# Performance work log

Measured on AMD Instinct MI355X. Metric: run time of the kernel, lower is better.

Reference implementation:

```python
import jax, jax.numpy as jnp
import numpy as np

# ---- shape constants (d_data=1, expand_factor=1) ----
B, L, DD = 32, 8192, 1
M, NL = 3, 2                      # 3 Mamba control nets, n_layers=2 each
DM = 4 * DD                       # mamba d_model = 4*d_data
DI = DM                           # d_inner = expand_factor * d_model
NS = 16                           # d_state
KC = 4                            # d_conv
DR = max(1, -(-DM // 16))         # dt_rank = ceil(d_model/16)
DT = 1e-4                         # forward scalar arg dt (fixed python float)
TAU = 1000.0
SMOOTH = int(round(0.001 / DT))   # smooth_len/dt = 10

# 9-point (8th order) central finite-difference coefficients for f' (no 1/dt)
_C1 = [1/280, -4/105, 1/5, -4/5, 0.0, 4/5, -1/5, 4/105, -1/280]

def deriv_approx_dy(x):
    Lp = x.shape[1] - 8
    return sum(c * x[:, k:k + Lp, :] for k, c in enumerate(_C1) if c != 0.0)

def smooth(x, k):
    # centered box filter, same output length (via cumsum sliding window)
    if k <= 1:
        return x
    xp = jnp.pad(x, ((0, 0), ((k - 1) // 2 + 1, k // 2), (0, 0)))
    c = jnp.cumsum(xp, axis=1)
    return (c[:, k:, :] - c[:, :-k, :]) / k

def rmsnorm(x, w):
    return x * jax.lax.rsqrt(jnp.mean(x * x, -1, keepdims=True) + 1e-5) * w

def causal_conv(u, w, b):
    # depthwise causal conv == torch Conv1d(groups=DI, padding=KC-1)[..., :L]
    Lc = u.shape[1]
    up = jnp.pad(u, ((0, 0), (KC - 1, 0), (0, 0)))
    y = sum(up[:, j:j + Lc, :] * w[:, j] for j in range(KC))
    return y + b

def selective_scan(u, delta, A, Bm, Cm, Dp):
    # u, delta: [b,l,di]; A: [di,ns]; Bm, Cm: [b,l,ns]; Dp: [di]
    dA = jnp.exp(delta[..., None] * A)                         # [b,l,di,ns]
    dBu = delta[..., None] * Bm[:, :, None, :] * u[..., None]  # [b,l,di,ns]
    def step(h, xs):
        a, bu = xs
        h = a * h + bu
        return h, h
    h0 = jnp.zeros((u.shape[0], DI, NS), u.dtype)
    _, hs = jax.lax.scan(step, h0, (jnp.moveaxis(dA, 1, 0), jnp.moveaxis(dBu, 1, 0)))
    hs = jnp.moveaxis(hs, 0, 1)                                # [b,l,di,ns]
    return jnp.einsum('bldn,bln->bld', hs, Cm) + u * Dp

def _run_mamba(x_in, m, in_proj_w, conv_w, conv_b, x_proj_w,
               dt_proj_w, dt_proj_b, A_log, D_param, norm_w, out_proj_w):
    h = x_in
    for l in range(NL):
        hn = rmsnorm(h, norm_w[m, l])
        xz = hn @ in_proj_w[m, l].T                            # [b,l,2*di]
        xc, res = jnp.split(xz, 2, axis=-1)
        xc = jax.nn.silu(causal_conv(xc, conv_w[m, l], conv_b[m, l]))
        dbc = xc @ x_proj_w[m, l].T
        dtr, Bm, Cm = dbc[..., :DR], dbc[..., DR:DR + NS], dbc[..., DR + NS:]
        delta = jax.nn.softplus(dtr @ dt_proj_w[m, l].T + dt_proj_b[m, l])
        A = -jnp.exp(A_log[m, l])
        y = selective_scan(xc, delta, A, Bm, Cm, D_param[m, l])
        y = y * jax.nn.silu(res)
        h = y @ out_proj_w[m, l].T + h                         # residual block
    return h

def _forward(x, in_proj_w, conv_w, conv_b, x_proj_w, dt_proj_w, dt_proj_b,
             A_log, D_param, norm_w, out_proj_w, omega_w, omega_b,
             gamma_w, gamma_b, d_w, d_b, b_param):
    xdot = deriv_approx_dy(x)                                  # [B, L-8, DD]
    z = jnp.concatenate([x[:, 4:-4, :], xdot], axis=-1)        # [B, L', 2]
    x_in = jnp.concatenate([z, jnp.flip(z, axis=1)], axis=-1)  # [B, L', 4]
    args = (in_proj_w, conv_w, conv_b, x_proj_w, dt_proj_w, dt_proj_b,
            A_log, D_param, norm_w, out_proj_w)
    omegaC = _run_mamba(x_in, 0, *args)
    gammaC = _run_mamba(x_in, 1, *args)
    dC = _run_mamba(x_in, 2, *args)
    b = jax.nn.relu(b_param) / TAU
    d = jax.nn.relu(dC @ d_w.T + d_b)
    omega = omegaC @ omega_w.T + omega_b
    gamma = (gammaC @ gamma_w.T + gamma_b) / TAU
    d = smooth(jnp.abs(d), SMOOTH)
    omega = smooth(jnp.abs(omega), SMOOTH)
    gamma = smooth(gamma, SMOOTH)
    z = jnp.concatenate([z[:, :, :-1], z[:, :, -1:] / DT], axis=-1)
    z1, z2 = z[:, :, :1], z[:, :, 1:]
    yhat = -omega ** 2 * z1 + gamma * z2 - b * (z1 ** 2) * z2 - d
    def pen(t):
        # torch.var(dim=1) is unbiased -> ddof=1
        return jnp.mean(jnp.var(jnp.diff(t, axis=1)[:, 1:, :], axis=1, ddof=1))
    penalty = (pen(omega) + pen(gamma) + pen(d)) / 3.0
    controls = jnp.concatenate([omegaC, gammaC, dC], axis=-1)
    return yhat, controls, penalty

def setup_inputs():
    key = jax.random.key(0)
    ks = jax.random.split(key, 16)
    f32 = jnp.float32
    def nrm(k, shape, s=0.1):
        return s * jax.random.normal(k, shape, f32)
    x = jax.random.normal(ks[0], (B, L, DD), f32)
    A_log = jnp.log(jnp.broadcast_to(jnp.arange(1, NS + 1, dtype=f32), (M, NL, DI, NS)))
    return {
        "x": x,
        "in_proj_w": nrm(ks[1], (M, NL, 2 * DI, DM)),
        "conv_w": nrm(ks[2], (M, NL, DI, KC)),
        "conv_b": nrm(ks[3], (M, NL, DI)),
        "x_proj_w": nrm(ks[4], (M, NL, DR + 2 * NS, DI)),
        "dt_proj_w": nrm(ks[5], (M, NL, DI, DR)),
        "dt_proj_b": nrm(ks[6], (M, NL, DI)),
        "A_log": A_log,
        "D_param": jnp.ones((M, NL, DI), f32),
        "norm_w": jnp.ones((M, NL, DM), f32),
        "out_proj_w": nrm(ks[7], (M, NL, DM, DI)),
        "omega_w": nrm(ks[8], (DD, DM)),
        "omega_b": nrm(ks[9], (DD,)),
        "gamma_w": nrm(ks[10], (DD, DM)),
        "gamma_b": nrm(ks[11], (DD,)),
        "d_w": nrm(ks[12], (DD, DM)),
        "d_b": nrm(ks[13], (DD,)),
        "b_param": jax.random.uniform(ks[14], (1,), f32),
    }

def reference(x, in_proj_w, conv_w, conv_b, x_proj_w, dt_proj_w, dt_proj_b,
              A_log, D_param, norm_w, out_proj_w, omega_w, omega_b,
              gamma_w, gamma_b, d_w, d_b, b_param):
    return _forward(x, in_proj_w, conv_w, conv_b, x_proj_w, dt_proj_w, dt_proj_b,
                    A_log, D_param, norm_w, out_proj_w, omega_w, omega_b,
                    gamma_w, gamma_b, d_w, d_b, b_param)
```

## Files before the change

### kernel.cpp

```cpp
#include <hip/hip_runtime.h>
#include <math.h>

#define Bn_   32
#define Ln_   8192
#define LCn   8184
#define NLn   2
#define NCHn  341
#define CHn   24
#define NGn   24

static constexpr long N_BL = (long)Bn_ * LCn;

static constexpr long OFF_H    = 0;
static constexpr long OFF_REC  = 12*N_BL;
static constexpr long OFF_YB   = 36*N_BL;
static constexpr long OFF_RAW  = OFF_REC;
static constexpr long OFF_PART = OFF_REC + 3*N_BL;

#define L2E_  1.4426950408889634f
#define LN2_  0.6931471805599453f
#define EXP2_(x) __builtin_amdgcn_exp2f(x)
#define LOG2_(x) __builtin_amdgcn_logf(x)

__device__ __forceinline__ float si_(float v) {
    float e = EXP2_(-v * L2E_);
    return v * __builtin_amdgcn_rcpf(1.f + e);
}

__device__ __forceinline__ float sel4(float4 v, int d) {
    return (d & 2) ? ((d & 1) ? v.w : v.z) : ((d & 1) ? v.y : v.x);
}

__device__ __forceinline__ float rowsum16(float p) {
    p += __int_as_float(__builtin_amdgcn_update_dpp(0, __float_as_int(p), 0x128, 0xF, 0xF, true));
    p += __int_as_float(__builtin_amdgcn_update_dpp(0, __float_as_int(p), 0x124, 0xF, 0xF, true));
    p += __int_as_float(__builtin_amdgcn_update_dpp(0, __float_as_int(p), 0x122, 0xF, 0xF, true));
    p += __int_as_float(__builtin_amdgcn_update_dpp(0, __float_as_int(p), 0x121, 0xF, 0xF, true));
    return p;
}

__device__ __forceinline__ float4 compute_xin(const float* __restrict__ xb, int p) {
    const float c0 = 1.f/280.f, c1 = -4.f/105.f, c2 = 0.2f, c3 = -0.8f,
                c5 = 0.8f, c6 = -0.2f, c7 = 4.f/105.f, c8 = -1.f/280.f;
    float xd  = c0*xb[p]   + c1*xb[p+1] + c2*xb[p+2] + c3*xb[p+3]
              + c5*xb[p+5] + c6*xb[p+6] + c7*xb[p+7] + c8*xb[p+8];
    int tf = LCn - 1 - p;
    float xdf = c0*xb[tf]   + c1*xb[tf+1] + c2*xb[tf+2] + c3*xb[tf+3]
              + c5*xb[tf+5] + c6*xb[tf+6] + c7*xb[tf+7] + c8*xb[tf+8];
    float4 v; v.x = xb[p+4]; v.y = xd; v.z = xb[tf+4]; v.w = xdf;
    return v;
}

__device__ __forceinline__ float4 rms_xproj(float4 hv, const float* __restrict__ wn,
                                            const float* __restrict__ W) {
    float ms = (hv.x*hv.x + hv.y*hv.y + hv.z*hv.z + hv.w*hv.w)*0.25f + 1e-5f;
    float rs = __builtin_amdgcn_rsqf(ms);
    float hn0 = hv.x*rs*wn[0], hn1 = hv.y*rs*wn[1];
    float hn2 = hv.z*rs*wn[2], hn3 = hv.w*rs*wn[3];
    float4 o;
    o.x = W[0]*hn0  + W[1]*hn1  + W[2]*hn2  + W[3]*hn3;
    o.y = W[4]*hn0  + W[5]*hn1  + W[6]*hn2  + W[7]*hn3;
    o.z = W[8]*hn0  + W[9]*hn1  + W[10]*hn2 + W[11]*hn3;
    o.w = W[12]*hn0 + W[13]*hn1 + W[14]*hn2 + W[15]*hn3;
    return o;
}

__device__ __forceinline__ void conv_lg_store(const float4* xp, int k, int ml,
                                              const float* __restrict__ cw,
                                              const float* __restrict__ cbv,
                                              const float* __restrict__ xpw,
                                              const float* __restrict__ dtw,
                                              const float* __restrict__ dtb,
                                              float* __restrict__ rp) {
    const float* wc = cw  + ml*16;
    const float* bc = cbv + ml*4;
    float acc0 = bc[0], acc1 = bc[1], acc2 = bc[2], acc3 = bc[3];
#pragma unroll
    for (int j = 0; j < 4; j++) {
        float4 xv = xp[k + j];
        acc0 = fmaf(xv.x, wc[0*4+j], acc0);
        acc1 = fmaf(xv.y, wc[1*4+j], acc1);
        acc2 = fmaf(xv.z, wc[2*4+j], acc2);
        acc3 = fmaf(xv.w, wc[3*4+j], acc3);
    }
    float4 o;
    o.x = si_(acc0); o.y = si_(acc1); o.z = si_(acc2); o.w = si_(acc3);
    const float* P = xpw + (long)ml*33*4;
    float dtr = o.x*P[0] + o.y*P[1] + o.z*P[2] + o.w*P[3];
    const float* dwv = dtw + ml*4;
    const float* dbv = dtb + ml*4;
    float4 lg;
    lg.x = LOG2_(1.f + EXP2_(fmaf(dtr, dwv[0], dbv[0]) * L2E_));
    lg.y = LOG2_(1.f + EXP2_(fmaf(dtr, dwv[1], dbv[1]) * L2E_));
    lg.z = LOG2_(1.f + EXP2_(fmaf(dtr, dwv[2], dbv[2]) * L2E_));
    lg.w = LOG2_(1.f + EXP2_(fmaf(dtr, dwv[3], dbv[3]) * L2E_));
    *(float4*)rp       = o;
    *(float4*)(rp + 4) = lg;
}

__global__ __launch_bounds__(256)
void k_pre0(const float* __restrict__ x,
            const float* __restrict__ ipw, const float* __restrict__ cw,
            const float* __restrict__ cbv, const float* __restrict__ nw,
            const float* __restrict__ xpw, const float* __restrict__ dtw,
            const float* __restrict__ dtb, float* __restrict__ rec) {
    __shared__ float4 xp[259];
    int blk = blockIdx.x;
    int m = blk >> 10, bb = (blk >> 5) & 31, tile = blk & 31;
    int ml = m*NLn;
    int t0 = tile << 8, k = threadIdx.x;
    int t  = t0 + k;
    const float* xb = x + (long)bb*Ln_;
    const float* W  = ipw + (long)ml*32;
    const float* wn = nw  + ml*4;
    auto G = [&](int p) -> float4 {
        float4 o; o.x = o.y = o.z = o.w = 0.f;
        if (p >= 0 && p < LCn) o = rms_xproj(compute_xin(xb, p), wn, W);
        return o;
    };
    xp[k + 3] = G(t);
    if (k < 3) xp[k] = G(t0 + k - 3);
    __syncthreads();
    if (t >= LCn) return;
    conv_lg_store(xp, k, ml, cw, cbv, xpw, dtw, dtb,
                  rec + ((long)m*N_BL + (long)bb*LCn + t)*8);
}

__global__ __launch_bounds__(256)
void k_mid(const float* __restrict__ x, const float* __restrict__ yb,
           float* __restrict__ hout,
           const float* __restrict__ ipw, const float* __restrict__ cw,
           const float* __restrict__ cbv, const float* __restrict__ nw,
           const float* __restrict__ xpw, const float* __restrict__ dtw,
           const float* __restrict__ dtb, const float* __restrict__ opw,
           float* __restrict__ rec) {
    __shared__ float4 xp[259];
    int blk = blockIdx.x;
    int m = blk >> 10, bb = (blk >> 5) & 31, tile = blk & 31;
    int ml0 = m*NLn, ml1 = ml0 + 1;
    int t0 = tile << 8, k = threadIdx.x;
    int t  = t0 + k;
    const float* xb  = x + (long)bb*Ln_;
    const float* wn0 = nw + ml0*4;
    const float* Wr  = ipw + (long)(ml0*8 + 4)*4;
    const float* O   = opw + ml0*16;
    const float* wn1 = nw + ml1*4;
    const float* W1  = ipw + (long)ml1*32;
    auto H = [&](int p) -> float4 {
        float4 hv = compute_xin(xb, p);
        float ms = (hv.x*hv.x + hv.y*hv.y + hv.z*hv.z + hv.w*hv.w)*0.25f + 1e-5f;
        float rs = __builtin_amdgcn_rsqf(ms);
        float hn0 = hv.x*rs*wn0[0], hn1 = hv.y*rs*wn0[1];
        float hn2 = hv.z*rs*wn0[2], hn3 = hv.w*rs*wn0[3];
        float4 yv = *(const float4*)(yb + ((long)m*N_BL + (long)bb*LCn + p)*4);
        float g0 = yv.x * si_(Wr[0]*hn0  + Wr[1]*hn1  + Wr[2]*hn2  + Wr[3]*hn3);
        float g1 = yv.y * si_(Wr[4]*hn0  + Wr[5]*hn1  + Wr[6]*hn2  + Wr[7]*hn3);
        float g2 = yv.z * si_(Wr[8]*hn0  + Wr[9]*hn1  + Wr[10]*hn2 + Wr[11]*hn3);
        float g3 = yv.w * si_(Wr[12]*hn0 + Wr[13]*hn1 + Wr[14]*hn2 + Wr[15]*hn3);
        float4 o;
        o.x = O[0]*g0  + O[1]*g1  + O[2]*g2  + O[3]*g3  + hv.x;
        o.y = O[4]*g0  + O[5]*g1  + O[6]*g2  + O[7]*g3  + hv.y;
        o.z = O[8]*g0  + O[9]*g1  + O[10]*g2 + O[11]*g3 + hv.z;
        o.w = O[12]*g0 + O[13]*g1 + O[14]*g2 + O[15]*g3 + hv.w;
        return o;
    };
    float4 zf; zf.x = zf.y = zf.z = zf.w = 0.f;
    if (t < LCn) {
        float4 hnew = H(t);
        *(float4*)(hout + ((long)m*N_BL + (long)bb*LCn + t)*4) = hnew;
        xp[k + 3] = rms_xproj(hnew, wn1, W1);
    } else {
        xp[k + 3] = zf;
    }
    if (k < 3) {
        int p = t0 + k - 3;
        xp[k] = (p >= 0) ? rms_xproj(H(p), wn1, W1) : zf;
    }
    __syncthreads();
    if (t >= LCn) return;
    conv_lg_store(xp, k, ml1, cw, cbv, xpw, dtw, dtb,
                  rec + ((long)m*N_BL + (long)bb*LCn + t)*8);
}

__global__ __launch_bounds__(256, 8)
void k_scanB(const float* __restrict__ rec, int l,
             const float* __restrict__ xpw, const float* __restrict__ Alog,
             float* __restrict__ Ap, float* __restrict__ Sv) {
    int wid  = blockIdx.x*4 + (threadIdx.x >> 6);
    int lane = threadIdx.x & 63;
    int chunk = wid % NCHn;
    int g     = wid / NCHn;
    int m = g >> 3;
    int s = lane >> 4, n = lane & 15;
    int bb = (g & 7)*4 + s;
    int ml = m*NLn + l;
    const float* P  = xpw + (long)ml*33*4;
    const float* PB = P + (1+n)*4;
    float pb0 = PB[0]*LN2_, pb1 = PB[1]*LN2_, pb2 = PB[2]*LN2_, pb3 = PB[3]*LN2_;
    const float* AL = Alog + (long)ml*64 + n;
    float4 Av;
    Av.x = -EXP2_(AL[0]  * L2E_);
    Av.y = -EXP2_(AL[16] * L2E_);
    Av.z = -EXP2_(AL[32] * L2E_);
    Av.w = -EXP2_(AL[48] * L2E_);
    const float* rb = rec + ((long)m*N_BL + (long)bb*LCn)*8;
    int t0 = chunk*CHn;
    float4 ap; ap.x = ap.y = ap.z = ap.w = 1.f;
    float4 sv; sv.x = sv.y = sv.z = sv.w = 0.f;
#pragma unroll 4
    for (int t = t0; t < t0 + CHn; t++) {
        float4 u  = *(const float4*)(rb + (long)t*8);
        float4 lg = *(const float4*)(rb + (long)t*8 + 4);
        float Bv = u.x*pb0 + u.y*pb1 + u.z*pb2 + u.w*pb3;
        float4 a;
        a.x = EXP2_(lg.x * Av.x); a.y = EXP2_(lg.y * Av.y);
        a.z = EXP2_(lg.z * Av.z); a.w = EXP2_(lg.w * Av.w);
        sv.x = fmaf(a.x, sv.x, lg.x*u.x*Bv);
        sv.y = fmaf(a.y, sv.y, lg.y*u.y*Bv);
        sv.z = fmaf(a.z, sv.z, lg.z*u.z*Bv);
        sv.w = fmaf(a.w, sv.w, lg.w*u.w*Bv);
        ap.x *= a.x; ap.y *= a.y; ap.z *= a.z; ap.w *= a.w;
    }
    long ci = (((long)g*NCHn + chunk)*64 + lane)*4;
    *(float4*)(Ap + ci) = ap;
    *(float4*)(Sv + ci) = sv;
}

#define SCANC_G 8
__global__ __launch_bounds__(256)
void k_scanC(const float* __restrict__ Ap, float* __restrict__ Sv) {
    int g   = blockIdx.x;
    int tid = threadIdx.x;
    long base = (long)g*NCHn*256 + tid;
    const int NFULL = NCHn / SCANC_G;
    float h = 0.f;
    float ca[SCANC_G], cs[SCANC_G], na[SCANC_G], ns[SCANC_G];
#pragma unroll
    for (int j = 0; j < SCANC_G; j++) {
        ca[j] = Ap[base + (long)j*256];
        cs[j] = Sv[base + (long)j*256];
    }
    for (int grp = 0; grp < NFULL; grp++) {
        long gb = base + (long)grp*SCANC_G*256;
        if (grp + 1 < NFULL) {
            long nb = gb + (long)SCANC_G*256;
#pragma unroll
            for (int j = 0; j < SCANC_G; j++) {
                na[j] = Ap[nb + (long)j*256];
                ns[j] = Sv[nb + (long)j*256];
            }
        }
#pragma unroll
        for (int j = 0; j < SCANC_G; j++) {
            Sv[gb + (long)j*256] = h;
            h = fmaf(ca[j], h, cs[j]);
        }
#pragma unroll
        for (int j = 0; j < SCANC_G; j++) { ca[j] = na[j]; cs[j] = ns[j]; }
    }
    for (int cc = NFULL*SCANC_G; cc < NCHn; cc++) {
        long ci = base + (long)cc*256;
        float a = Ap[ci];
        float s = Sv[ci];
        Sv[ci] = h;
        h = fmaf(a, h, s);
    }
}

__global__ __launch_bounds__(256, 8)
void k_scanD(const float* __restrict__ rec, float* __restrict__ yb, int l,
             const float* __restrict__ xpw, const float* __restrict__ Alog,
             const float* __restrict__ H0, const float* __restrict__ Dp) {
    int wid  = blockIdx.x*4 + (threadIdx.x >> 6);
    int lane = threadIdx.x & 63;
    int chunk = wid % NCHn;
    int g     = wid / NCHn;
    int m = g >> 3;
    int s = lane >> 4, n = lane & 15;
    int bb = (g & 7)*4 + s;
    int ml = m*NLn + l;
    const float* P  = xpw + (long)ml*33*4;
    const float* PB = P + (1+n)*4;
    float pb0 = PB[0]*LN2_, pb1 = PB[1]*LN2_, pb2 = PB[2]*LN2_, pb3 = PB[3]*LN2_;
    const float* PC = P + (17+n)*4;
    float pc0 = PC[0], pc1 = PC[1], pc2 = PC[2], pc3 = PC[3];
    const float* AL = Alog + (long)ml*64 + n;
    float4 Av;
    Av.x = -EXP2_(AL[0]  * L2E_);
    Av.y = -EXP2_(AL[16] * L2E_);
    Av.z = -EXP2_(AL[32] * L2E_);
    Av.w = -EXP2_(AL[48] * L2E_);
    float Dd = Dp[ml*4 + (n & 3)];
    float4 h = *(const float4*)(H0 + (((long)g*NCHn + chunk)*64 + lane)*4);
    const float* rb = rec + ((long)m*N_BL + (long)bb*LCn)*8;
    float* ym = yb + ((long)m*N_BL + (long)bb*LCn)*4;
    int t0 = chunk*CHn;
#pragma unroll 4
    for (int t = t0; t < t0 + CHn; t++) {
        float4 u  = *(const float4*)(rb + (long)t*8);
        float4 lg = *(const float4*)(rb + (long)t*8 + 4);
        float Bv = u.x*pb0 + u.y*pb1 + u.z*pb2 + u.w*pb3;
        float Cv = u.x*pc0 + u.y*pc1 + u.z*pc2 + u.w*pc3;
        float4 a;
        a.x = EXP2_(lg.x * Av.x); a.y = EXP2_(lg.y * Av.y);
        a.z = EXP2_(lg.z * Av.z); a.w = EXP2_(lg.w * Av.w);
        h.x = fmaf(a.x, h.x, lg.x*u.x*Bv);
        h.y = fmaf(a.y, h.y, lg.y*u.y*Bv);
        h.z = fmaf(a.z, h.z, lg.z*u.z*Bv);
        h.w = fmaf(a.w, h.w, lg.w*u.w*Bv);
        float px = rowsum16(h.x * Cv);
        float py = rowsum16(h.y * Cv);
        float pz = rowsum16(h.z * Cv);
        float pw = rowsum16(h.w * Cv);
        if (n < 4) {
            float out = (n & 2) ? ((n & 1) ? pw : pz) : ((n & 1) ? py : px);
            float ud  = sel4(u, n);
            ym[(long)t*4 + n] = fmaf(ud, Dd, out);
        }
    }
}

__global__ void k_postHead(const float* __restrict__ hin,
                           const float* __restrict__ yb,
                           const float* __restrict__ ipw, const float* __restrict__ nw,
                           const float* __restrict__ opw,
                           const float* __restrict__ ww, const float* __restrict__ wb,
                           const float* __restrict__ gw, const float* __restrict__ gb,
                           const float* __restrict__ dw, const float* __restrict__ dbp,
                           float* __restrict__ raw, float* __restrict__ dout) {
    long r = (long)blockIdx.x * 256 + threadIdx.x;
    if (r >= N_BL) return;
    float4 om[3];
#pragma unroll
    for (int m = 0; m < 3; m++) {
        int ml = m*NLn + 1;
        float4 hv = *(const float4*)(hin + (long)m*4*N_BL + r*4);
        float ms = (hv.x*hv.x + hv.y*hv.y + hv.z*hv.z + hv.w*hv.w)*0.25f + 1e-5f;
        float rs = __builtin_amdgcn_rsqf(ms);
        const float* wn = nw + ml*4;
        float hn0 = hv.x*rs*wn[0], hn1 = hv.y*rs*wn[1];
        float hn2 = hv.z*rs*wn[2], hn3 = hv.w*rs*wn[3];
        const float* W = ipw + (long)(ml*8 + 4)*4;
        float4 yv = *(const float4*)(yb + ((long)m*N_BL + r)*4);
        float g0 = yv.x * si_(W[0]*hn0  + W[1]*hn1  + W[2]*hn2  + W[3]*hn3);
        float g1 = yv.y * si_(W[4]*hn0  + W[5]*hn1  + W[6]*hn2  + W[7]*hn3);
        float g2 = yv.z * si_(W[8]*hn0  + W[9]*hn1  + W[10]*hn2 + W[11]*hn3);
        float g3 = yv.w * si_(W[12]*hn0 + W[13]*hn1 + W[14]*hn2 + W[15]*hn3);
        const float* O = opw + ml*16;
        float4 o;
        o.x = O[0]*g0  + O[1]*g1  + O[2]*g2  + O[3]*g3  + hv.x;
        o.y = O[4]*g0  + O[5]*g1  + O[6]*g2  + O[7]*g3  + hv.y;
        o.z = O[8]*g0  + O[9]*g1  + O[10]*g2 + O[11]*g3 + hv.z;
        o.w = O[12]*g0 + O[13]*g1 + O[14]*g2 + O[15]*g3 + hv.w;
        om[m] = o;
    }
    float4* c = (float4*)(dout + N_BL + r*12);
    c[0] = om[0]; c[1] = om[1]; c[2] = om[2];
    raw[r]          = om[0].x*ww[0] + om[0].y*ww[1] + om[0].z*ww[2] + om[0].w*ww[3] + wb[0];
    raw[N_BL + r]   = (om[1].x*gw[0] + om[1].y*gw[1] + om[1].z*gw[2] + om[1].w*gw[3] + gb[0]) / 1000.0f;
    raw[2*N_BL + r] = fmaxf(om[2].x*dw[0] + om[2].y*dw[1] + om[2].z*dw[2] + om[2].w*dw[3] + dbp[0], 0.f);
}

__global__ __launch_bounds__(256)
void k_smoothpen(const float* __restrict__ x, const float* __restrict__ raw,
                 const float* __restrict__ bp, float* __restrict__ dout,
                 double* __restrict__ part) {
    int b    = blockIdx.x >> 5;
    int tile = blockIdx.x & 31;
    int k    = threadIdx.x;
    int t0   = tile << 8;
    int t    = t0 + k;
    __shared__ float so_[257], sg_[257], sd_[257];
    const float* ro = raw + (long)b*LCn;
    const float* rg = raw + N_BL   + (long)b*LCn;
    const float* rd = raw + 2*N_BL + (long)b*LCn;
    auto smo3 = [&](int tt, float& o, float& g, float& d) {
        o = g = d = 0.f;
        if (tt < 0 || tt >= LCn) return;
        int lo = max(tt - 4, 0), hi = min(tt + 5, LCn - 1);
        for (int q = lo; q <= hi; q++) {
            o += fabsf(ro[q]); g += rg[q]; d += fabsf(rd[q]);
        }
        o *= 0.1f; g *= 0.1f; d *= 0.1f;
    };
    float so, sg, sd;
    smo3(t, so, sg, sd);
    so_[k] = so; sg_[k] = sg; sd_[k] = sd;
    if (k == 0) {
        float a, bq, cq;
        smo3(t0 + 256, a, bq, cq);
        so_[256] = a; sg_[256] = bq; sd_[256] = cq;
    }
    __syncthreads();
    if (t < LCn) {
        const float* xb = x + (long)b * Ln_;
        const float c0 = 1.f/280.f, c1 = -4.f/105.f, c2 = 0.2f, c3 = -0.8f,
                    c5 = 0.8f, c6 = -0.2f, c7 = 4.f/105.f, c8 = -1.f/280.f;
        float xd  = c0*xb[t]   + c1*xb[t+1] + c2*xb[t+2] + c3*xb[t+3]
                  + c5*xb[t+5] + c6*xb[t+6] + c7*xb[t+7] + c8*xb[t+8];
        float z1 = xb[t+4];
        float z2 = xd / 0.0001f;
        float bq = fmaxf(bp[0], 0.f) / 1000.0f;
        dout[(long)b*LCn + t] = -so*so*z1 + sg*z2 - bq*z1*z1*z2 - sd;
    }
    double v[6] = {0,0,0,0,0,0};
    if (t >= 1 && t <= LCn - 2) {
        double go = (double)so_[k+1] - (double)so_[k];
        double gg = (double)sg_[k+1] - (double)sg_[k];
        double gd = (double)sd_[k+1] - (double)sd_[k];
        v[0] = go; v[1] = go*go;
        v[2] = gg; v[3] = gg*gg;
        v[4] = gd; v[5] = gd*gd;
    }
#pragma unroll
    for (int j = 0; j < 6; j++) {
        for (int off = 32; off > 0; off >>= 1)
            v[j] += __shfl_down(v[j], off, 64);
    }
    __shared__ double wsum[4][6];
    int w = threadIdx.x >> 6;
    if ((threadIdx.x & 63) == 0) {
#pragma unroll
        for (int j = 0; j < 6; j++) wsum[w][j] = v[j];
    }
    __syncthreads();
    if (threadIdx.x == 0) {
        double s[6];
#pragma unroll
        for (int j = 0; j < 6; j++)
            s[j] = wsum[0][j] + wsum[1][j] + wsum[2][j] + wsum[3][j];
        long pb = (((long)0*32 + b)*32 + tile)*2;
        part[pb]   = s[0]; part[pb+1] = s[1];
        pb = (((long)1*32 + b)*32 + tile)*2;
        part[pb]   = s[2]; part[pb+1] = s[3];
        pb = (((long)2*32 + b)*32 + tile)*2;
        part[pb]   = s[4]; part[pb+1] = s[5];
    }
}

__global__ void k_pen2(const double* __restrict__ part, float* __restrict__ pout) {
    int tid = threadIdx.x;
    double var = 0.0;
    if (tid < 96) {
        int which = tid / 32, b = tid % 32;
        double su = 0.0, s2 = 0.0;
        for (int tl = 0; tl < 32; tl++) {
            const double* p = part + (((long)which*32 + b)*32 + tl)*2;
            su += p[0]; s2 += p[1];
        }
        const double N = (double)(LCn - 2);
        var = (s2 - su*su/N) / (N - 1.0);
    }
    __shared__ double sh[128];
    sh[tid] = var;
    __syncthreads();
    for (int o = 64; o > 0; o >>= 1) {
        if (tid < o) sh[tid] += sh[tid + o];
        __syncthreads();
    }
    if (tid == 0) pout[0] = (float)(sh[0] / 96.0);
}

extern "C" void kernel_launch(void* const* d_in, const int* in_sizes, int n_in,
                              void* d_out, int out_size, void* d_ws, size_t ws_size,
                              hipStream_t stream) {
    const float* x    = (const float*)d_in[0];
    const float* ipw  = (const float*)d_in[1];
    const float* cw   = (const float*)d_in[2];
    const float* cbv  = (const float*)d_in[3];
    const float* xpw  = (const float*)d_in[4];
    const float* dtw  = (const float*)d_in[5];
    const float* dtb  = (const float*)d_in[6];
    const float* Alog = (const float*)d_in[7];
    const float* Dp   = (const float*)d_in[8];
    const float* nw   = (const float*)d_in[9];
    const float* opw  = (const float*)d_in[10];
    const float* ww   = (const float*)d_in[11];
    const float* wb   = (const float*)d_in[12];
    const float* gw   = (const float*)d_in[13];
    const float* gb   = (const float*)d_in[14];
    const float* dw   = (const float*)d_in[15];
    const float* dbp  = (const float*)d_in[16];
    const float* bp   = (const float*)d_in[17];

    float* ws   = (float*)d_ws;
    float* h    = ws + OFF_H;
    float* rec  = ws + OFF_REC;
    float* yb   = ws + OFF_YB;
    float* ap   = yb;
    float* raw  = ws + OFF_RAW;
    double* part = (double*)(ws + OFF_PART);
    float* dout = (float*)d_out;
    float* sv  = dout + 4*N_BL;

    hipLaunchKernelGGL(k_pre0, dim3(3072), dim3(256), 0, stream,
                       x, ipw, cw, cbv, nw, xpw, dtw, dtb, rec);
    hipLaunchKernelGGL(k_scanB, dim3(2046), dim3(256), 0, stream,
                       rec, 0, xpw, Alog, ap, sv);
    hipLaunchKernelGGL(k_scanC, dim3(NGn), dim3(256), 0, stream, ap, sv);
    hipLaunchKernelGGL(k_scanD, dim3(2046), dim3(256), 0, stream,
                       rec, yb, 0, xpw, Alog, sv, Dp);
    hipLaunchKernelGGL(k_mid, dim3(3072), dim3(256), 0, stream,
                       x, yb, h, ipw, cw, cbv, nw, xpw, dtw, dtb, opw, rec);
    hipLaunchKernelGGL(k_scanB, dim3(2046), dim3(256), 0, stream,
                       rec, 1, xpw, Alog, ap, sv);
    hipLaunchKernelGGL(k_scanC, dim3(NGn), dim3(256), 0, stream, ap, sv);
    hipLaunchKernelGGL(k_scanD, dim3(2046), dim3(256), 0, stream,
                       rec, yb, 1, xpw, Alog, sv, Dp);
    hipLaunchKernelGGL(k_postHead, dim3(1023), dim3(256), 0, stream,
                       h, yb, ipw, nw, opw, ww, wb, gw, gb, dw, dbp, raw, dout);
    hipLaunchKernelGGL(k_smoothpen, dim3(1024), dim3(256), 0, stream,
                       x, raw, bp, dout, part);
    hipLaunchKernelGGL(k_pen2, dim3(1), dim3(128), 0, stream, part, dout + 13*N_BL);
}
```

Baseline: 177.8 us.

## Fuse chunk-carry scan into scan pass via last-block atomic, fuse head with smoothing

The chunk-carry scan kernel is folded into the per-chunk scan kernel. A global atomic counter per group lets the last finishing block run the sequential carry propagation. Chunking changes to 328 chunks of 25 steps so there are no leftover chunks, with a bound check on the final chunk. The post-head projection is fused into the smoothing/penalty kernel, which recomputes a 10-element halo in shared memory instead of writing and re-reading an intermediate raw buffer. This removes two launches per layer and one global round trip, at the cost of atomics, fences and some redundant halo compute.

```diff
diff --git a/kernel.cpp b/kernel.cpp
--- a/kernel.cpp
+++ b/kernel.cpp
@@ -5,17 +5,18 @@
 #define Ln_   8192
 #define LCn   8184
 #define NLn   2
-#define NCHn  341
-#define CHn   24
+#define NCHn  328
+#define CHn   25
 #define NGn   24
+#define BLKPG 82
 
 static constexpr long N_BL = (long)Bn_ * LCn;
+static constexpr long NCAR = (long)NGn * NCHn * 256;
 
 static constexpr long OFF_H    = 0;
 static constexpr long OFF_REC  = 12*N_BL;
 static constexpr long OFF_YB   = 36*N_BL;
-static constexpr long OFF_RAW  = OFF_REC;
-static constexpr long OFF_PART = OFF_REC + 3*N_BL;
+static constexpr long OFF_PART = OFF_REC;
 
 #define L2E_  1.4426950408889634f
 #define LN2_  0.6931471805599453f
@@ -103,7 +104,9 @@
             const float* __restrict__ ipw, const float* __restrict__ cw,
             const float* __restrict__ cbv, const float* __restrict__ nw,
             const float* __restrict__ xpw, const float* __restrict__ dtw,
-            const float* __restrict__ dtb, float* __restrict__ rec) {
+            const float* __restrict__ dtb, float* __restrict__ rec,
+            int* __restrict__ gcnt) {
+    if (blockIdx.x == 0 && threadIdx.x < NGn) gcnt[threadIdx.x] = 0;
     __shared__ float4 xp[259];
     int blk = blockIdx.x;
     int m = blk >> 10, bb = (blk >> 5) & 31, tile = blk & 31;
@@ -133,7 +136,8 @@
            const float* __restrict__ cbv, const float* __restrict__ nw,
            const float* __restrict__ xpw, const float* __restrict__ dtw,
            const float* __restrict__ dtb, const float* __restrict__ opw,
-           float* __restrict__ rec) {
+           float* __restrict__ rec, int* __restrict__ gcnt) {
+    if (blockIdx.x == 0 && threadIdx.x < NGn) gcnt[threadIdx.x] = 0;
     __shared__ float4 xp[259];
     int blk = blockIdx.x;
     int m = blk >> 10, bb = (blk >> 5) & 31, tile = blk & 31;
@@ -182,10 +186,12 @@
                   rec + ((long)m*N_BL + (long)bb*LCn + t)*8);
 }
 
+#define SCANC_G 8
 __global__ __launch_bounds__(256, 8)
-void k_scanB(const float* __restrict__ rec, int l,
-             const float* __restrict__ xpw, const float* __restrict__ Alog,
-             float* __restrict__ Ap, float* __restrict__ Sv) {
+void k_scanBC(const float* __restrict__ rec, int l,
+              const float* __restrict__ xpw, const float* __restrict__ Alog,
+              float* __restrict__ Ap, float* __restrict__ Sv,
+              int* __restrict__ gcnt) {
     int wid  = blockIdx.x*4 + (threadIdx.x >> 6);
     int lane = threadIdx.x & 63;
     int chunk = wid % NCHn;
@@ -204,11 +210,11 @@
     Av.z = -EXP2_(AL[32] * L2E_);
     Av.w = -EXP2_(AL[48] * L2E_);
     const float* rb = rec + ((long)m*N_BL + (long)bb*LCn)*8;
-    int t0 = chunk*CHn;
+    int t0 = chunk*CHn, t1 = min(t0 + CHn, LCn);
     float4 ap; ap.x = ap.y = ap.z = ap.w = 1.f;
     float4 sv; sv.x = sv.y = sv.z = sv.w = 0.f;
 #pragma unroll 4
-    for (int t = t0; t < t0 + CHn; t++) {
+    for (int t = t0; t < t1; t++) {
         float4 u  = *(const float4*)(rb + (long)t*8);
         float4 lg = *(const float4*)(rb + (long)t*8 + 4);
         float Bv = u.x*pb0 + u.y*pb1 + u.z*pb2 + u.w*pb3;
@@ -224,12 +230,14 @@
     long ci = (((long)g*NCHn + chunk)*64 + lane)*4;
     *(float4*)(Ap + ci) = ap;
     *(float4*)(Sv + ci) = sv;
-}
-
-#define SCANC_G 8
-__global__ __launch_bounds__(256)
-void k_scanC(const float* __restrict__ Ap, float* __restrict__ Sv) {
-    int g   = blockIdx.x;
+    __threadfence();
+    __syncthreads();
+    __shared__ int lastf;
+    if (threadIdx.x == 0)
+        lastf = (atomicAdd(&gcnt[g], 1) == BLKPG - 1);
+    __syncthreads();
+    if (!lastf) return;
+    __threadfence();
     int tid = threadIdx.x;
     long base = (long)g*NCHn*256 + tid;
     const int NFULL = NCHn / SCANC_G;
@@ -258,13 +266,7 @@
 #pragma unroll
         for (int j = 0; j < SCANC_G; j++) { ca[j] = na[j]; cs[j] = ns[j]; }
     }
-    for (int cc = NFULL*SCANC_G; cc < NCHn; cc++) {
-        long ci = base + (long)cc*256;
-        float a = Ap[ci];
-        float s = Sv[ci];
-        Sv[ci] = h;
-        h = fmaf(a, h, s);
-    }
+    if (tid == 0) gcnt[g] = 0;
 }
 
 __global__ __launch_bounds__(256, 8)
@@ -294,9 +296,9 @@
     float4 h = *(const float4*)(H0 + (((long)g*NCHn + chunk)*64 + lane)*4);
     const float* rb = rec + ((long)m*N_BL + (long)bb*LCn)*8;
     float* ym = yb + ((long)m*N_BL + (long)bb*LCn)*4;
-    int t0 = chunk*CHn;
+    int t0 = chunk*CHn, t1 = min(t0 + CHn, LCn);
 #pragma unroll 4
-    for (int t = t0; t < t0 + CHn; t++) {
+    for (int t = t0; t < t1; t++) {
         float4 u  = *(const float4*)(rb + (long)t*8);
         float4 lg = *(const float4*)(rb + (long)t*8 + 4);
         float Bv = u.x*pb0 + u.y*pb1 + u.z*pb2 + u.w*pb3;
@@ -320,78 +322,80 @@
     }
 }
 
-__global__ void k_postHead(const float* __restrict__ hin,
-                           const float* __restrict__ yb,
-                           const float* __restrict__ ipw, const float* __restrict__ nw,
-                           const float* __restrict__ opw,
-                           const float* __restrict__ ww, const float* __restrict__ wb,
-                           const float* __restrict__ gw, const float* __restrict__ gb,
-                           const float* __restrict__ dw, const float* __restrict__ dbp,
-                           float* __restrict__ raw, float* __restrict__ dout) {
-    long r = (long)blockIdx.x * 256 + threadIdx.x;
-    if (r >= N_BL) return;
-    float4 om[3];
-#pragma unroll
-    for (int m = 0; m < 3; m++) {
-        int ml = m*NLn + 1;
-        float4 hv = *(const float4*)(hin + (long)m*4*N_BL + r*4);
-        float ms = (hv.x*hv.x + hv.y*hv.y + hv.z*hv.z + hv.w*hv.w)*0.25f + 1e-5f;
-        float rs = __builtin_amdgcn_rsqf(ms);
-        const float* wn = nw + ml*4;
-        float hn0 = hv.x*rs*wn[0], hn1 = hv.y*rs*wn[1];
-        float hn2 = hv.z*rs*wn[2], hn3 = hv.w*rs*wn[3];
-        const float* W = ipw + (long)(ml*8 + 4)*4;
-        float4 yv = *(const float4*)(yb + ((long)m*N_BL + r)*4);
-        float g0 = yv.x * si_(W[0]*hn0  + W[1]*hn1  + W[2]*hn2  + W[3]*hn3);
-        float g1 = yv.y * si_(W[4]*hn0  + W[5]*hn1  + W[6]*hn2  + W[7]*hn3);
-        float g2 = yv.z * si_(W[8]*hn0  + W[9]*hn1  + W[10]*hn2 + W[11]*hn3);
-        float g3 = yv.w * si_(W[12]*hn0 + W[13]*hn1 + W[14]*hn2 + W[15]*hn3);
-        const float* O = opw + ml*16;
-        float4 o;
-        o.x = O[0]*g0  + O[1]*g1  + O[2]*g2  + O[3]*g3  + hv.x;
-        o.y = O[4]*g0  + O[5]*g1  + O[6]*g2  + O[7]*g3  + hv.y;
-        o.z = O[8]*g0  + O[9]*g1  + O[10]*g2 + O[11]*g3 + hv.z;
-        o.w = O[12]*g0 + O[13]*g1 + O[14]*g2 + O[15]*g3 + hv.w;
-        om[m] = o;
-    }
-    float4* c = (float4*)(dout + N_BL + r*12);
-    c[0] = om[0]; c[1] = om[1]; c[2] = om[2];
-    raw[r]          = om[0].x*ww[0] + om[0].y*ww[1] + om[0].z*ww[2] + om[0].w*ww[3] + wb[0];
-    raw[N_BL + r]   = (om[1].x*gw[0] + om[1].y*gw[1] + om[1].z*gw[2] + om[1].w*gw[3] + gb[0]) / 1000.0f;
-    raw[2*N_BL + r] = fmaxf(om[2].x*dw[0] + om[2].y*dw[1] + om[2].z*dw[2] + om[2].w*dw[3] + dbp[0], 0.f);
-}
-
 __global__ __launch_bounds__(256)
-void k_smoothpen(const float* __restrict__ x, const float* __restrict__ raw,
-                 const float* __restrict__ bp, float* __restrict__ dout,
-                 double* __restrict__ part) {
+void k_tail(const float* __restrict__ x, const float* __restrict__ hin,
+            const float* __restrict__ yb,
+            const float* __restrict__ ipw, const float* __restrict__ nw,
+            const float* __restrict__ opw,
+            const float* __restrict__ ww, const float* __restrict__ wb,
+            const float* __restrict__ gw, const float* __restrict__ gb,
+            const float* __restrict__ dw, const float* __restrict__ dbp,
+            const float* __restrict__ bp,
+            float* __restrict__ dout, double* __restrict__ part) {
     int b    = blockIdx.x >> 5;
     int tile = blockIdx.x & 31;
     int k    = threadIdx.x;
     int t0   = tile << 8;
-    int t    = t0 + k;
+    __shared__ float ro_[266], rg_[266], rd_[266];
     __shared__ float so_[257], sg_[257], sd_[257];
-    const float* ro = raw + (long)b*LCn;
-    const float* rg = raw + N_BL   + (long)b*LCn;
-    const float* rd = raw + 2*N_BL + (long)b*LCn;
-    auto smo3 = [&](int tt, float& o, float& g, float& d) {
+    auto rawcalc = [&](int e) {
+        int t = t0 - 4 + e;
+        float vo = 0.f, vg = 0.f, vd = 0.f;
+        if (t >= 0 && t < LCn) {
+            long r = (long)b*LCn + t;
+            float4 om[3];
+#pragma unroll
+            for (int m = 0; m < 3; m++) {
+                int ml = m*NLn + 1;
+                float4 hv = *(const float4*)(hin + (long)m*4*N_BL + r*4);
+                float ms = (hv.x*hv.x + hv.y*hv.y + hv.z*hv.z + hv.w*hv.w)*0.25f + 1e-5f;
+                float rs = __builtin_amdgcn_rsqf(ms);
+                const float* wn = nw + ml*4;
+                float hn0 = hv.x*rs*wn[0], hn1 = hv.y*rs*wn[1];
+                float hn2 = hv.z*rs*wn[2], hn3 = hv.w*rs*wn[3];
+                const float* W = ipw + (long)(ml*8 + 4)*4;
+                float4 yv = *(const float4*)(yb + ((long)m*N_BL + r)*4);
+                float g0 = yv.x * si_(W[0]*hn0  + W[1]*hn1  + W[2]*hn2  + W[3]*hn3);
+                float g1 = yv.y * si_(W[4]*hn0  + W[5]*hn1  + W[6]*hn2  + W[7]*hn3);
+                float g2 = yv.z * si_(W[8]*hn0  + W[9]*hn1  + W[10]*hn2 + W[11]*hn3);
+                float g3 = yv.w * si_(W[12]*hn0 + W[13]*hn1 + W[14]*hn2 + W[15]*hn3);
+                const float* O = opw + ml*16;
+                float4 o;
+                o.x = O[0]*g0  + O[1]*g1  + O[2]*g2  + O[3]*g3  + hv.x;
+                o.y = O[4]*g0  + O[5]*g1  + O[6]*g2  + O[7]*g3  + hv.y;
+                o.z = O[8]*g0  + O[9]*g1  + O[10]*g2 + O[11]*g3 + hv.z;
+                o.w = O[12]*g0 + O[13]*g1 + O[14]*g2 + O[15]*g3 + hv.w;
+                om[m] = o;
+            }
+            float4* c = (float4*)(dout + N_BL + r*12);
+            c[0] = om[0]; c[1] = om[1]; c[2] = om[2];
+            vo = om[0].x*ww[0] + om[0].y*ww[1] + om[0].z*ww[2] + om[0].w*ww[3] + wb[0];
+            vg = (om[1].x*gw[0] + om[1].y*gw[1] + om[1].z*gw[2] + om[1].w*gw[3] + gb[0]) / 1000.0f;
+            vd = fmaxf(om[2].x*dw[0] + om[2].y*dw[1] + om[2].z*dw[2] + om[2].w*dw[3] + dbp[0], 0.f);
+        }
+        ro_[e] = vo; rg_[e] = vg; rd_[e] = vd;
+    };
+    rawcalc(k);
+    if (k < 10) rawcalc(k + 256);
+    __syncthreads();
+    auto smo = [&](int kk, float& o, float& g, float& d) {
         o = g = d = 0.f;
-        if (tt < 0 || tt >= LCn) return;
-        int lo = max(tt - 4, 0), hi = min(tt + 5, LCn - 1);
-        for (int q = lo; q <= hi; q++) {
-            o += fabsf(ro[q]); g += rg[q]; d += fabsf(rd[q]);
+#pragma unroll
+        for (int j = 0; j < 10; j++) {
+            o += fabsf(ro_[kk + j]); g += rg_[kk + j]; d += fabsf(rd_[kk + j]);
         }
         o *= 0.1f; g *= 0.1f; d *= 0.1f;
     };
     float so, sg, sd;
-    smo3(t, so, sg, sd);
+    smo(k, so, sg, sd);
     so_[k] = so; sg_[k] = sg; sd_[k] = sd;
     if (k == 0) {
-        float a, bq, cq;
-        smo3(t0 + 256, a, bq, cq);
-        so_[256] = a; sg_[256] = bq; sd_[256] = cq;
-    }
-    __syncthreads();
+        float a1, b1, c1;
+        smo(256, a1, b1, c1);
+        so_[256] = a1; sg_[256] = b1; sd_[256] = c1;
+    }
+    __syncthreads();
+    int t = t0 + k;
     if (t < LCn) {
         const float* xb = x + (long)b * Ln_;
         const float c0 = 1.f/280.f, c1 = -4.f/105.f, c2 = 0.2f, c3 = -0.8f,
@@ -425,16 +429,16 @@
     }
     __syncthreads();
     if (threadIdx.x == 0) {
-        double s[6];
+        double sarr[6];
 #pragma unroll
         for (int j = 0; j < 6; j++)
-            s[j] = wsum[0][j] + wsum[1][j] + wsum[2][j] + wsum[3][j];
+            sarr[j] = wsum[0][j] + wsum[1][j] + wsum[2][j] + wsum[3][j];
         long pb = (((long)0*32 + b)*32 + tile)*2;
-        part[pb]   = s[0]; part[pb+1] = s[1];
+        part[pb]   = sarr[0]; part[pb+1] = sarr[1];
         pb = (((long)1*32 + b)*32 + tile)*2;
-        part[pb]   = s[2]; part[pb+1] = s[3];
+        part[pb]   = sarr[2]; part[pb+1] = sarr[3];
         pb = (((long)2*32 + b)*32 + tile)*2;
-        part[pb]   = s[4]; part[pb+1] = s[5];
+        part[pb]   = sarr[4]; part[pb+1] = sarr[5];
     }
 }
 
@@ -488,28 +492,24 @@
     float* rec  = ws + OFF_REC;
     float* yb   = ws + OFF_YB;
     float* ap   = yb;
-    float* raw  = ws + OFF_RAW;
     double* part = (double*)(ws + OFF_PART);
     float* dout = (float*)d_out;
-    float* sv  = dout + 4*N_BL;
+    float* sv   = dout + 4*N_BL;
+    int*   gcnt = (int*)(sv + 2020000);
 
     hipLaunchKernelGGL(k_pre0, dim3(3072), dim3(256), 0, stream,
-                       x, ipw, cw, cbv, nw, xpw, dtw, dtb, rec);
-    hipLaunchKernelGGL(k_scanB, dim3(2046), dim3(256), 0, stream,
-                       rec, 0, xpw, Alog, ap, sv);
-    hipLaunchKernelGGL(k_scanC, dim3(NGn), dim3(256), 0, stream, ap, sv);
-    hipLaunchKernelGGL(k_scanD, dim3(2046), dim3(256), 0, stream,
+                       x, ipw, cw, cbv, nw, xpw, dtw, dtb, rec, gcnt);
+    hipLaunchKernelGGL(k_scanBC, dim3(NGn*NCHn/4), dim3(256), 0, stream,
+                       rec, 0, xpw, Alog, ap, sv, gcnt);
+    hipLaunchKernelGGL(k_scanD, dim3(NGn*NCHn/4), dim3(256), 0, stream,
                        rec, yb, 0, xpw, Alog, sv, Dp);
     hipLaunchKernelGGL(k_mid, dim3(3072), dim3(256), 0, stream,
-                       x, yb, h, ipw, cw, cbv, nw, xpw, dtw, dtb, opw, rec);
-    hipLaunchKernelGGL(k_scanB, dim3(2046), dim3(256), 0, stream,
-                       rec, 1, xpw, Alog, ap, sv);
-    hipLaunchKernelGGL(k_scanC, dim3(NGn), dim3(256), 0, stream, ap, sv);
-    hipLaunchKernelGGL(k_scanD, dim3(2046), dim3(256), 0, stream,
+                       x, yb, h, ipw, cw, cbv, nw, xpw, dtw, dtb, opw, rec, gcnt);
+    hipLaunchKernelGGL(k_scanBC, dim3(NGn*NCHn/4), dim3(256), 0, stream,
+                       rec, 1, xpw, Alog, ap, sv, gcnt);
+    hipLaunchKernelGGL(k_scanD, dim3(NGn*NCHn/4), dim3(256), 0, stream,
                        rec, yb, 1, xpw, Alog, sv, Dp);
-    hipLaunchKernelGGL(k_postHead, dim3(1023), dim3(256), 0, stream,
-                       h, yb, ipw, nw, opw, ww, wb, gw, gb, dw, dbp, raw, dout);
-    hipLaunchKernelGGL(k_smoothpen, dim3(1024), dim3(256), 0, stream,
-                       x, raw, bp, dout, part);
+    hipLaunchKernelGGL(k_tail, dim3(1024), dim3(256), 0, stream,
+                       x, h, yb, ipw, nw, opw, ww, wb, gw, gb, dw, dbp, bp, dout, part);
     hipLaunchKernelGGL(k_pen2, dim3(1), dim3(128), 0, stream, part, dout + 13*N_BL);
 }
```

Measured after the change: 659.2 us. 3.71x slower.
